# Kernel tuning notes

Hardware: AMD Instinct MI355X
Metric: run time of the kernel (lower is better)

The kernel has to match this reference:

```python
import jax, jax.numpy as jnp
import numpy as np

B, L, H, S, IN = 64, 64, 128, 64, 16  # batch, embedding_seq_len, hidden, seq_num, input_size


def setup_inputs() -> dict:
    key = jax.random.key(0)
    k = jax.random.split(key, 8)
    trip = jax.random.normal(k[0], (B, 256, IN), dtype=jnp.float32)
    valid_len = jax.random.randint(k[1], (B,), 0, 256)
    embedding = jax.random.normal(k[2], (B, L, H), dtype=jnp.float32)
    # gates: Linear(2H -> 4H), xavier-uniform weight
    lim_g = float(np.sqrt(6.0 / (2 * H + 4 * H)))
    W_gates = jax.random.uniform(k[3], (2 * H, 4 * H), minval=-lim_g, maxval=lim_g, dtype=jnp.float32)
    b_gates = jax.random.uniform(k[4], (4 * H,), minval=-1.0 / np.sqrt(2 * H), maxval=1.0 / np.sqrt(2 * H), dtype=jnp.float32)
    # linear: Linear(H -> input_size)
    lim_l = float(np.sqrt(6.0 / (H + IN)))
    W_lin = jax.random.uniform(k[5], (H, IN), minval=-lim_l, maxval=lim_l, dtype=jnp.float32)
    b_lin = jax.random.uniform(k[6], (IN,), minval=-1.0 / np.sqrt(H), maxval=1.0 / np.sqrt(H), dtype=jnp.float32)
    return {"trip": trip, "valid_len": valid_len, "embedding": embedding,
            "W_gates": W_gates, "b_gates": b_gates, "W_lin": W_lin, "b_lin": b_lin}


def _gate_update(inp, c, W_gates, b_gates):
    g = inp @ W_gates + b_gates
    f, i, o, cand = jnp.split(g, 4, axis=-1)
    c_new = jax.nn.sigmoid(f) * c + jax.nn.sigmoid(i) * jnp.tanh(cand)  # broadcasts [B,1,H] vs [B,L,H] at step 0
    h_new = jax.nn.sigmoid(o) * jnp.tanh(c_new)
    return c_new, h_new


def reference(trip, valid_len, embedding, W_gates, b_gates, W_lin, b_lin):
    x = trip  # sampler pass-through
    b, l, h = embedding.shape
    c0 = jnp.zeros((b, l, h), dtype=embedding.dtype)
    h0 = jnp.zeros((b, l, h), dtype=embedding.dtype)
    # step 0: gates on [embedding[:, :1], h[:, :1]] -> [B,1,4H], broadcast update
    inp0 = jnp.concatenate([embedding[:, :1, :], h0[:, :1, :]], axis=-1)
    c1, h1 = _gate_update(inp0, c0, W_gates, b_gates)

    def step(carry, _):
        c, hh = carry
        inp = jnp.concatenate([c, hh], axis=-1)  # [B,L,2H]
        c_new, h_new = _gate_update(inp, c, W_gates, b_gates)
        return (c_new, h_new), c_new

    (_, _), cs = jax.lax.scan(step, (c1, h1), None, length=S - 1)  # cs: [S-1,B,L,H]
    c_all = jnp.concatenate([c1[None], cs], axis=0)          # [S,B,L,H]
    c_all = jnp.transpose(c_all, (1, 0, 2, 3)).reshape(b, S * l, h)  # cat along dim=-2
    out = c_all @ W_lin + b_lin  # [B, S*L, IN]
    return (x, out)
```

## Files before the change

### kernel.cpp

```cpp
#include <hip/hip_runtime.h>

typedef _Float16 half2_t __attribute__((ext_vector_type(2)));

#define NBATCH 64
#define HDIM   128
#define NSTEP  64
#define NIN    16
#define HISTP  132

__device__ __forceinline__ float sigf(float x) { return 1.f / (1.f + __expf(-x)); }

__device__ __forceinline__ unsigned int h2u(half2_t h) {
    union { half2_t h; unsigned int u; } x; x.h = h; return x.u;
}
__device__ __forceinline__ half2_t u2h(unsigned int u) {
    union { half2_t h; unsigned int u; } x; x.u = u; return x.h;
}

__global__ __launch_bounds__(256) void copy_trip_k(const float4* __restrict__ src,
                                                   float4* __restrict__ dst) {
    int i = blockIdx.x * 256 + threadIdx.x;
    dst[i] = src[i];
}

__global__ __launch_bounds__(1024) void recur_k(
    const float* __restrict__ emb, const float* __restrict__ Wg,
    const float* __restrict__ bg,  const float* __restrict__ Wl,
    const float* __restrict__ bl,  float* __restrict__ proj_ws) {
    __shared__ __align__(16) unsigned int pack_s[2][128];
    __shared__ float gpart[2][512];
    __shared__ float hist[NSTEP * HISTP];
    __shared__ float Wl_s[HDIM * NIN];
    __shared__ float bg_s[512];

    const int b = blockIdx.x, t = threadIdx.x;
    const int j = t & 511, kh = t >> 9;

    unsigned int Wr[64];
    #pragma unroll
    for (int k = 0; k < 64; ++k) {
        float w0 = Wg[(kh * 128 + 2 * k + 0) * 512 + j];
        float w1 = Wg[(kh * 128 + 2 * k + 1) * 512 + j];
        half2_t hp = { (_Float16)w0, (_Float16)w1 };
        Wr[k] = h2u(hp);
    }

    if (t < 512) bg_s[t] = bg[t];
    for (int i = t; i < HDIM * NIN; i += 1024) Wl_s[i] = Wl[i];
    if (t < 64) {
        float e0 = emb[b * (64 * HDIM) + 2 * t + 0];
        float e1 = emb[b * (64 * HDIM) + 2 * t + 1];
        half2_t hp = { (_Float16)e0, (_Float16)e1 };
        pack_s[0][t] = h2u(hp);
    } else if (t < 128) {
        pack_s[0][t] = 0u;
    }
    float c_reg = 0.f;
    __syncthreads();

    for (int s = 0; s < NSTEP; ++s) {
        const uint4* p4 = (const uint4*)&pack_s[s & 1][kh * 64];
        float a0 = 0.f, a1 = 0.f;
        #pragma unroll
        for (int q = 0; q < 16; ++q) {
            uint4 u = p4[q];
            a0 = __builtin_amdgcn_fdot2(u2h(u.x), u2h(Wr[4 * q + 0]), a0, false);
            a1 = __builtin_amdgcn_fdot2(u2h(u.y), u2h(Wr[4 * q + 1]), a1, false);
            a0 = __builtin_amdgcn_fdot2(u2h(u.z), u2h(Wr[4 * q + 2]), a0, false);
            a1 = __builtin_amdgcn_fdot2(u2h(u.w), u2h(Wr[4 * q + 3]), a1, false);
        }
        gpart[kh][j] = a0 + a1;
        __syncthreads();

        if (t < HDIM) {
            float fg = sigf(gpart[0][t]       + gpart[1][t]       + bg_s[t]);
            float ig = sigf(gpart[0][128 + t] + gpart[1][128 + t] + bg_s[128 + t]);
            float og = sigf(gpart[0][256 + t] + gpart[1][256 + t] + bg_s[256 + t]);
            float cd = tanhf(gpart[0][384 + t] + gpart[1][384 + t] + bg_s[384 + t]);
            float c_new = fg * c_reg + ig * cd;
            float h_new = og * tanhf(c_new);
            c_reg = c_new;
            hist[s * HISTP + t] = c_new;
            float c_o = __shfl_xor(c_new, 1);
            float h_o = __shfl_xor(h_new, 1);
            if ((t & 1) == 0) {
                half2_t cp = { (_Float16)c_new, (_Float16)c_o };
                half2_t hp = { (_Float16)h_new, (_Float16)h_o };
                int nb = (s + 1) & 1;
                pack_s[nb][(t >> 1)]      = h2u(cp);
                pack_s[nb][64 + (t >> 1)] = h2u(hp);
            }
        }
        __syncthreads();
    }

    {
        int s = t >> 4, i = t & 15;
        float acc = bl[i];
        const float4* c4 = (const float4*)&hist[s * HISTP];
        #pragma unroll 8
        for (int h4 = 0; h4 < HDIM / 4; ++h4) {
            float4 cv = c4[h4];
            int h = h4 * 4;
            acc = fmaf(cv.x, Wl_s[(h + 0) * NIN + i], acc);
            acc = fmaf(cv.y, Wl_s[(h + 1) * NIN + i], acc);
            acc = fmaf(cv.z, Wl_s[(h + 2) * NIN + i], acc);
            acc = fmaf(cv.w, Wl_s[(h + 3) * NIN + i], acc);
        }
        proj_ws[b * 1024 + t] = acc;
    }
}

__global__ __launch_bounds__(256) void expand_k(const float* __restrict__ proj_ws,
                                                float* __restrict__ out) {
    int blk = blockIdx.x;
    int t = threadIdx.x;
    const float4* pj = (const float4*)(proj_ws + blk * 16);
    float4 v = pj[t & 3];
    float4* ob = (float4*)(out + (size_t)blk * 1024);
    ob[t] = v;
}

extern "C" void kernel_launch(void* const* d_in, const int* in_sizes, int n_in,
                              void* d_out, int out_size, void* d_ws, size_t ws_size,
                              hipStream_t stream) {
    const float* trip = (const float*)d_in[0];
    const float* emb  = (const float*)d_in[2];
    const float* Wg   = (const float*)d_in[3];
    const float* bgp  = (const float*)d_in[4];
    const float* Wlp  = (const float*)d_in[5];
    const float* blp  = (const float*)d_in[6];
    float* out = (float*)d_out;
    float* proj_ws = (float*)d_ws;

    copy_trip_k<<<256, 256, 0, stream>>>((const float4*)trip, (float4*)out);
    recur_k<<<NBATCH, 1024, 0, stream>>>(emb, Wg, bgp, Wlp, blp, proj_ws);
    expand_k<<<NBATCH * NSTEP, 256, 0, stream>>>(proj_ws, out + 262144);
}
```

Baseline: 92.83 us.

## Keep gate weights in AGPRs and broadcast packed state via readlane

Stores each thread's 64 packed fp16 weight pairs in accumulator registers (AGPRs) through inline asm instead of ordinary VGPRs. Each step, every lane loads two packed state words from LDS, and the values are broadcast with v_readlane instead of every lane reading 16 uint4 from shared memory. The state buffer is now single-buffered, which relies on the two barriers per step for ordering. The intent is to relieve VGPR pressure at 1024 threads and cut LDS traffic in the serial recurrence, at the cost of extra accvgpr_read and readlane instructions.

```diff
diff --git a/kernel.cpp b/kernel.cpp
--- a/kernel.cpp
+++ b/kernel.cpp
@@ -23,11 +23,27 @@
     dst[i] = src[i];
 }
 
+#define PUTW(K) { \
+    float w0_ = Wg[(base + 2*(K)) * 512 + j]; \
+    float w1_ = Wg[(base + 2*(K) + 1) * 512 + j]; \
+    half2_t hp_ = { (_Float16)w0_, (_Float16)w1_ }; \
+    unsigned int u_ = h2u(hp_); \
+    asm volatile("v_accvgpr_write_b32 a" #K ", %0" :: "v"(u_) : "a" #K); }
+
+#define SQ(Q, K0, K1) { \
+    unsigned int sx_ = (unsigned int)__builtin_amdgcn_readlane((int)vx, lbase + (Q)); \
+    unsigned int sy_ = (unsigned int)__builtin_amdgcn_readlane((int)vy, lbase + (Q)); \
+    unsigned int wa_, wb_; \
+    asm volatile("v_accvgpr_read_b32 %0, a" #K0 : "=v"(wa_)); \
+    asm volatile("v_accvgpr_read_b32 %0, a" #K1 : "=v"(wb_)); \
+    acc0 = __builtin_amdgcn_fdot2(u2h(sx_), u2h(wa_), acc0, false); \
+    acc1 = __builtin_amdgcn_fdot2(u2h(sy_), u2h(wb_), acc1, false); }
+
 __global__ __launch_bounds__(1024) void recur_k(
     const float* __restrict__ emb, const float* __restrict__ Wg,
     const float* __restrict__ bg,  const float* __restrict__ Wl,
     const float* __restrict__ bl,  float* __restrict__ proj_ws) {
-    __shared__ __align__(16) unsigned int pack_s[2][128];
+    __shared__ __align__(16) unsigned int pack_s[128];
     __shared__ float gpart[2][512];
     __shared__ float hist[NSTEP * HISTP];
     __shared__ float Wl_s[HDIM * NIN];
@@ -35,15 +51,18 @@
 
     const int b = blockIdx.x, t = threadIdx.x;
     const int j = t & 511, kh = t >> 9;
+    const int lane = t & 63;
+    const int lbase = kh << 5;
+    const int base = kh * 128;
 
-    unsigned int Wr[64];
-    #pragma unroll
-    for (int k = 0; k < 64; ++k) {
-        float w0 = Wg[(kh * 128 + 2 * k + 0) * 512 + j];
-        float w1 = Wg[(kh * 128 + 2 * k + 1) * 512 + j];
-        half2_t hp = { (_Float16)w0, (_Float16)w1 };
-        Wr[k] = h2u(hp);
-    }
+    PUTW(0)  PUTW(1)  PUTW(2)  PUTW(3)  PUTW(4)  PUTW(5)  PUTW(6)  PUTW(7)
+    PUTW(8)  PUTW(9)  PUTW(10) PUTW(11) PUTW(12) PUTW(13) PUTW(14) PUTW(15)
+    PUTW(16) PUTW(17) PUTW(18) PUTW(19) PUTW(20) PUTW(21) PUTW(22) PUTW(23)
+    PUTW(24) PUTW(25) PUTW(26) PUTW(27) PUTW(28) PUTW(29) PUTW(30) PUTW(31)
+    PUTW(32) PUTW(33) PUTW(34) PUTW(35) PUTW(36) PUTW(37) PUTW(38) PUTW(39)
+    PUTW(40) PUTW(41) PUTW(42) PUTW(43) PUTW(44) PUTW(45) PUTW(46) PUTW(47)
+    PUTW(48) PUTW(49) PUTW(50) PUTW(51) PUTW(52) PUTW(53) PUTW(54) PUTW(55)
+    PUTW(56) PUTW(57) PUTW(58) PUTW(59) PUTW(60) PUTW(61) PUTW(62) PUTW(63)
 
     if (t < 512) bg_s[t] = bg[t];
     for (int i = t; i < HDIM * NIN; i += 1024) Wl_s[i] = Wl[i];
@@ -51,25 +70,27 @@
         float e0 = emb[b * (64 * HDIM) + 2 * t + 0];
         float e1 = emb[b * (64 * HDIM) + 2 * t + 1];
         half2_t hp = { (_Float16)e0, (_Float16)e1 };
-        pack_s[0][t] = h2u(hp);
+        pack_s[t] = h2u(hp);
     } else if (t < 128) {
-        pack_s[0][t] = 0u;
+        pack_s[t] = 0u;
     }
     float c_reg = 0.f;
     __syncthreads();
 
     for (int s = 0; s < NSTEP; ++s) {
-        const uint4* p4 = (const uint4*)&pack_s[s & 1][kh * 64];
-        float a0 = 0.f, a1 = 0.f;
-        #pragma unroll
-        for (int q = 0; q < 16; ++q) {
-            uint4 u = p4[q];
-            a0 = __builtin_amdgcn_fdot2(u2h(u.x), u2h(Wr[4 * q + 0]), a0, false);
-            a1 = __builtin_amdgcn_fdot2(u2h(u.y), u2h(Wr[4 * q + 1]), a1, false);
-            a0 = __builtin_amdgcn_fdot2(u2h(u.z), u2h(Wr[4 * q + 2]), a0, false);
-            a1 = __builtin_amdgcn_fdot2(u2h(u.w), u2h(Wr[4 * q + 3]), a1, false);
-        }
-        gpart[kh][j] = a0 + a1;
+        uint2 sv = *(const uint2*)((const char*)pack_s + lane * 8);
+        unsigned int vx = sv.x, vy = sv.y;
+
+        float acc0 = 0.f, acc1 = 0.f;
+        SQ(0,0,1)    SQ(1,2,3)    SQ(2,4,5)    SQ(3,6,7)
+        SQ(4,8,9)    SQ(5,10,11)  SQ(6,12,13)  SQ(7,14,15)
+        SQ(8,16,17)  SQ(9,18,19)  SQ(10,20,21) SQ(11,22,23)
+        SQ(12,24,25) SQ(13,26,27) SQ(14,28,29) SQ(15,30,31)
+        SQ(16,32,33) SQ(17,34,35) SQ(18,36,37) SQ(19,38,39)
+        SQ(20,40,41) SQ(21,42,43) SQ(22,44,45) SQ(23,46,47)
+        SQ(24,48,49) SQ(25,50,51) SQ(26,52,53) SQ(27,54,55)
+        SQ(28,56,57) SQ(29,58,59) SQ(30,60,61) SQ(31,62,63)
+        gpart[kh][j] = acc0 + acc1;
         __syncthreads();
 
         if (t < HDIM) {
@@ -86,9 +107,8 @@
             if ((t & 1) == 0) {
                 half2_t cp = { (_Float16)c_new, (_Float16)c_o };
                 half2_t hp = { (_Float16)h_new, (_Float16)h_o };
-                int nb = (s + 1) & 1;
-                pack_s[nb][(t >> 1)]      = h2u(cp);
-                pack_s[nb][64 + (t >> 1)] = h2u(hp);
+                pack_s[(t >> 1)]      = h2u(cp);
+                pack_s[64 + (t >> 1)] = h2u(hp);
             }
         }
         __syncthreads();
```

Result: slower. 188.4 us (+103.0%).
